# Optimization experiments

Measured on AMD Instinct MI355X. Metric: run time of the kernel, lower is better.

Reference implementation:

```python
import jax, jax.numpy as jnp
import numpy as np

N_NODES = 100000
N_EDGES = 1600000
IN_DIM, HID_DIM, OUT_DIM = 128, 128, 1


def gcn_conv(x, W, b, src, dst, n_nodes):
    """PyG-style GCNConv: add self-loops, symmetric D^-1/2 (A+I) D^-1/2 normalization.

    x: [N, F_in], W: [F_in, F_out], b: [F_out], src/dst: [E] int edge endpoints.
    """
    h = x @ W  # [N, F_out] transform first (as PyG does)
    # degree on A + I, counted over destination (symmetric graph assumption)
    ones = jnp.ones(src.shape[0], dtype=h.dtype)
    deg = jax.ops.segment_sum(ones, dst, num_segments=n_nodes) + 1.0  # +1 self loop
    dinv = jax.lax.rsqrt(deg)  # [N]
    norm = dinv[src] * dinv[dst]  # [E] edge normalization
    msg = h[src] * norm[:, None]  # [E, F_out] gather + scale
    agg = jax.ops.segment_sum(msg, dst, num_segments=n_nodes)  # scatter-add
    # self-loop contribution: norm_ii = dinv[i]^2
    out = agg + h * (dinv * dinv)[:, None]
    return out + b


def setup_inputs() -> dict:
    key = jax.random.key(0)
    k1, k2, k3, k4 = jax.random.split(key, 4)
    x = jax.random.normal(k1, (N_NODES, IN_DIM), dtype=jnp.float32)
    edge_index = jax.random.randint(k2, (2, N_EDGES), 0, N_NODES, dtype=jnp.int64)
    W1 = jax.random.normal(k3, (IN_DIM, HID_DIM), dtype=jnp.float32) * (1.0 / np.sqrt(IN_DIM))
    b1 = jnp.zeros((HID_DIM,), dtype=jnp.float32)
    W2 = jax.random.normal(k4, (HID_DIM, OUT_DIM), dtype=jnp.float32) * (1.0 / np.sqrt(HID_DIM))
    b2 = jnp.zeros((OUT_DIM,), dtype=jnp.float32)
    return {"x": x, "edge_index": edge_index, "W1": W1, "b1": b1, "W2": W2, "b2": b2}


def reference(x, edge_index, W1, b1, W2, b2):
    n = x.shape[0]
    src, dst = edge_index[0], edge_index[1]
    h = gcn_conv(x, W1, b1, src, dst, n)
    h = jax.nn.relu(h)
    # dropout(p=0.2) is identity at inference
    out = gcn_conv(h, W2, b2, src, dst, n)  # [N, 1]
    return out
```

## Files before the change

### kernel.cpp

```cpp
#include <hip/hip_runtime.h>

#define N_NODES 100000
#define N_EDGES 1600000
#define DIM 128

#define BSHIFT 8
#define BNODES 256
#define NBUCK 391
#define BCAP  4608
#define PCHUNK 4096
#define NB_PART ((N_EDGES + PCHUNK - 1) / PCHUNK)

#define GTILES 1563
#define GGRID  782

typedef short s16x8 __attribute__((ext_vector_type(8)));
typedef float f32x4 __attribute__((ext_vector_type(4)));

__device__ __forceinline__ unsigned short f2bf(float f) {
    unsigned u = __float_as_uint(f);
    u += 0x7fffu + ((u >> 16) & 1u);
    return (unsigned short)(u >> 16);
}
__device__ __forceinline__ float bflo(unsigned u) { return __uint_as_float(u << 16); }
__device__ __forceinline__ float bfhi(unsigned u) { return __uint_as_float(u & 0xffff0000u); }


__global__ void k_zero(int* __restrict__ gcur) {
    int t = blockIdx.x * blockDim.x + threadIdx.x;
    if (t < NBUCK) gcur[t] = t * BCAP;
}

__device__ __forceinline__ void part_body(char* smem, int bid,
                                          const int* __restrict__ src,
                                          const int* __restrict__ dst,
                                          int* __restrict__ gcur,
                                          int2* __restrict__ ebuf) {
    int* hist = (int*)smem;
    int* gbase = hist + NBUCK;
    int tid = threadIdx.x;
    long e0 = (long)bid * PCHUNK;
    int n = min(PCHUNK, (int)(N_EDGES - e0));
    for (int b = tid; b < NBUCK; b += 256) hist[b] = 0;
    __syncthreads();

    int mys[16], myd[16];
#pragma unroll
    for (int k = 0; k < 16; ++k) {
        int idx = k * 256 + tid;
        if (idx < n) {
            mys[k] = src[e0 + idx];
            myd[k] = dst[e0 + idx];
            atomicAdd(&hist[myd[k] >> BSHIFT], 1);
        } else {
            myd[k] = -1;
        }
    }
    __syncthreads();
    for (int b = tid; b < NBUCK; b += 256) {
        gbase[b] = hist[b] ? atomicAdd(&gcur[b], hist[b]) : 0;
        hist[b] = 0;
    }
    __syncthreads();
#pragma unroll
    for (int k = 0; k < 16; ++k) {
        if (myd[k] >= 0) {
            int b = myd[k] >> BSHIFT;
            int slot = gbase[b] + atomicAdd(&hist[b], 1);
            ebuf[slot] = make_int2(mys[k], myd[k]);
        }
    }
}

__device__ __forceinline__ void gemm_body(char* smem, int bid,
                                          const float* __restrict__ x,
                                          const float* __restrict__ W1,
                                          unsigned short* __restrict__ h1) {
    unsigned short* Wt = (unsigned short*)smem;
    int tid = threadIdx.x;
    for (int idx = tid; idx < DIM * DIM; idx += 256) {
        int k = idx >> 7, c = idx & 127;
        Wt[c * 128 + (k ^ ((c & 7) << 3))] = f2bf(W1[idx]);
    }
    __syncthreads();

    int wv = tid >> 6, lane = tid & 63;
    int g = lane >> 4, tl = lane & 15;
    unsigned short* cst = (unsigned short*)(smem + 32768 + wv * 4096);

    for (int tile = bid; tile < GTILES; tile += GGRID) {
        int rb = tile * 64 + wv * 16;
        if (rb >= N_NODES) continue;

        s16x8 afrag[4];
        const float* xrow = x + (size_t)(rb + tl) * DIM + g * 8;
#pragma unroll
        for (int kc = 0; kc < 4; ++kc) {
            float4 p0 = *(const float4*)(xrow + kc * 32);
            float4 p1 = *(const float4*)(xrow + kc * 32 + 4);
            s16x8 a;
            a[0] = (short)f2bf(p0.x); a[1] = (short)f2bf(p0.y);
            a[2] = (short)f2bf(p0.z); a[3] = (short)f2bf(p0.w);
            a[4] = (short)f2bf(p1.x); a[5] = (short)f2bf(p1.y);
            a[6] = (short)f2bf(p1.z); a[7] = (short)f2bf(p1.w);
            afrag[kc] = a;
        }

        f32x4 acc[8];
#pragma unroll
        for (int ct = 0; ct < 8; ++ct) acc[ct] = (f32x4)0.0f;
#pragma unroll
        for (int kc = 0; kc < 4; ++kc) {
#pragma unroll
            for (int ct = 0; ct < 8; ++ct) {
                int crow = ct * 16 + tl;
                int boff = crow * 256 + ((kc * 64 + g * 16) ^ ((crow & 7) << 4));
                s16x8 b = *(const s16x8*)((const char*)Wt + boff);
                acc[ct] = __builtin_amdgcn_mfma_f32_16x16x32_bf16(afrag[kc], b, acc[ct], 0, 0, 0);
            }
        }

#pragma unroll
        for (int ct = 0; ct < 8; ++ct) {
#pragma unroll
            for (int r = 0; r < 4; ++r) {
                float own = acc[ct][r];
                float oth = __shfl_xor(own, 1, 64);
                if ((lane & 1) == 0) {
                    unsigned pk = (unsigned)f2bf(own) | ((unsigned)f2bf(oth) << 16);
                    int row = g * 4 + r;
                    int col = ct * 16 + tl;
                    *(unsigned*)&cst[row * 128 + (col ^ (row << 3))] = pk;
                }
            }
        }
        asm volatile("s_waitcnt lgkmcnt(0)" ::: "memory");

        unsigned short* dstp = h1 + (size_t)rb * DIM;
#pragma unroll
        for (int c = 0; c < 4; ++c) {
            int row = c * 4 + g;
            uint4 v = *(const uint4*)&cst[row * 128 + ((tl ^ row) * 8)];
            *(uint4*)(dstp + c * 512 + lane * 8) = v;
        }
    }
}

__global__ __launch_bounds__(256) void k_part(const int* __restrict__ src,
                                              const int* __restrict__ dst,
                                              int* __restrict__ gcur,
                                              int2* __restrict__ ebuf) {
    __shared__ __align__(16) char smem[2 * NBUCK * 4 + 16];
    part_body(smem, blockIdx.x, src, dst, gcur, ebuf);
}

__global__ __launch_bounds__(256) void k_gemm(const float* __restrict__ x,
                                              const float* __restrict__ W1,
                                              unsigned short* __restrict__ h1) {
    __shared__ __align__(16) char smem[49152];
    gemm_body(smem, blockIdx.x, x, W1, h1);
}

__global__ __launch_bounds__(256) void k_pg(const int* __restrict__ src,
                                            const int* __restrict__ dst,
                                            int* __restrict__ gcur,
                                            int2* __restrict__ ebuf,
                                            const float* __restrict__ x,
                                            const float* __restrict__ W1,
                                            unsigned short* __restrict__ h1) {
    __shared__ __align__(16) char smem[49152];
    if (blockIdx.x < NB_PART) part_body(smem, blockIdx.x, src, dst, gcur, ebuf);
    else                      gemm_body(smem, blockIdx.x - NB_PART, x, W1, h1);
}

__global__ __launch_bounds__(256) void k_csrA(const int2* __restrict__ ebuf,
                                              const int* __restrict__ gcur,
                                              int* __restrict__ rp,
                                              int* __restrict__ cnt,
                                              float* __restrict__ dinv) {
    __shared__ int lcnt[BNODES];
    __shared__ int psum[BNODES];
    int b = blockIdx.x, t = threadIdx.x;
    int node0 = b << BSHIFT;
    lcnt[t] = 0;
    __syncthreads();
    int base = b * BCAP, end = gcur[b];
    for (int e = base + t; e < end; e += 256)
        atomicAdd(&lcnt[ebuf[e].y - node0], 1);
    __syncthreads();
    int c = lcnt[t];
    psum[t] = c;
    __syncthreads();
    for (int s = 1; s < 256; s <<= 1) {
        int u = (t >= s) ? psum[t - s] : 0;
        __syncthreads();
        psum[t] += u;
        __syncthreads();
    }
    int node = node0 + t;
    if (node < N_NODES) {
        rp[node] = base + psum[t] - c;
        cnt[node] = c;
        dinv[node] = rsqrtf((float)(c + 1));
    }
}

__global__ __launch_bounds__(256) void k_csrB(const int2* __restrict__ ebuf,
                                              const int* __restrict__ gcur,
                                              const int* __restrict__ rp,
                                              const float* __restrict__ dinv,
                                              int2* __restrict__ csrw) {
    __shared__ int lcur[BNODES];
    __shared__ float ldv[BNODES];
    int b = blockIdx.x, t = threadIdx.x;
    int node0 = b << BSHIFT;
    int base = b * BCAP, end = gcur[b];
    int node = node0 + t;
    if (node < N_NODES) { lcur[t] = rp[node] - base; ldv[t] = dinv[node]; }
    __syncthreads();
    int e = base + t;
    for (; e + 256 < end; e += 512) {
        int2 d0 = ebuf[e];
        int2 d1 = ebuf[e + 256];
        int l0 = d0.y - node0, l1 = d1.y - node0;
        float w0 = dinv[d0.x] * ldv[l0];
        float w1 = dinv[d1.x] * ldv[l1];
        int p0 = atomicAdd(&lcur[l0], 1);
        int p1 = atomicAdd(&lcur[l1], 1);
        csrw[base + p0] = make_int2(d0.x, __float_as_int(w0));
        csrw[base + p1] = make_int2(d1.x, __float_as_int(w1));
    }
    if (e < end) {
        int2 d0 = ebuf[e];
        int l0 = d0.y - node0;
        float w0 = dinv[d0.x] * ldv[l0];
        int p0 = atomicAdd(&lcur[l0], 1);
        csrw[base + p0] = make_int2(d0.x, __float_as_int(w0));
    }
}


__global__ __launch_bounds__(256) void k_agg1(const unsigned short* __restrict__ h1,
                                              const float* __restrict__ dinv,
                                              const int* __restrict__ rp,
                                              const int* __restrict__ cnt,
                                              const int2* __restrict__ csrw,
                                              const float* __restrict__ b1,
                                              const float* __restrict__ W2,
                                              float* __restrict__ z) {
    int lane = threadIdx.x & 63;
    int wv = threadIdx.x >> 6;
    int g = lane >> 4, tl = lane & 15;
    int i = blockIdx.x * 16 + wv * 4 + g;
    int c0 = tl * 8;
    float di = dinv[i];
    int beg = rp[i], end = beg + cnt[i];
    float a0 = 0.f, a1 = 0.f, a2 = 0.f, a3 = 0.f, a4 = 0.f, a5 = 0.f, a6 = 0.f, a7 = 0.f;
    const unsigned short* hbase = h1 + c0;

    int j = beg;
    for (; j + 4 <= end; j += 4) {
        int2 e0 = csrw[j];
        int2 e1 = csrw[j + 1];
        int2 e2 = csrw[j + 2];
        int2 e3 = csrw[j + 3];
        uint4 v0 = *(const uint4*)(hbase + (size_t)e0.x * DIM);
        uint4 v1 = *(const uint4*)(hbase + (size_t)e1.x * DIM);
        uint4 v2 = *(const uint4*)(hbase + (size_t)e2.x * DIM);
        uint4 v3 = *(const uint4*)(hbase + (size_t)e3.x * DIM);
        float w0 = __int_as_float(e0.y), w1 = __int_as_float(e1.y);
        float w2 = __int_as_float(e2.y), w3 = __int_as_float(e3.y);
        a0 = fmaf(bflo(v0.x), w0, a0); a1 = fmaf(bfhi(v0.x), w0, a1);
        a2 = fmaf(bflo(v0.y), w0, a2); a3 = fmaf(bfhi(v0.y), w0, a3);
        a4 = fmaf(bflo(v0.z), w0, a4); a5 = fmaf(bfhi(v0.z), w0, a5);
        a6 = fmaf(bflo(v0.w), w0, a6); a7 = fmaf(bfhi(v0.w), w0, a7);
        a0 = fmaf(bflo(v1.x), w1, a0); a1 = fmaf(bfhi(v1.x), w1, a1);
        a2 = fmaf(bflo(v1.y), w1, a2); a3 = fmaf(bfhi(v1.y), w1, a3);
        a4 = fmaf(bflo(v1.z), w1, a4); a5 = fmaf(bfhi(v1.z), w1, a5);
        a6 = fmaf(bflo(v1.w), w1, a6); a7 = fmaf(bfhi(v1.w), w1, a7);
        a0 = fmaf(bflo(v2.x), w2, a0); a1 = fmaf(bfhi(v2.x), w2, a1);
        a2 = fmaf(bflo(v2.y), w2, a2); a3 = fmaf(bfhi(v2.y), w2, a3);
        a4 = fmaf(bflo(v2.z), w2, a4); a5 = fmaf(bfhi(v2.z), w2, a5);
        a6 = fmaf(bflo(v2.w), w2, a6); a7 = fmaf(bfhi(v2.w), w2, a7);
        a0 = fmaf(bflo(v3.x), w3, a0); a1 = fmaf(bfhi(v3.x), w3, a1);
        a2 = fmaf(bflo(v3.y), w3, a2); a3 = fmaf(bfhi(v3.y), w3, a3);
        a4 = fmaf(bflo(v3.z), w3, a4); a5 = fmaf(bfhi(v3.z), w3, a5);
        a6 = fmaf(bflo(v3.w), w3, a6); a7 = fmaf(bfhi(v3.w), w3, a7);
    }
    for (; j < end; ++j) {
        int2 e0 = csrw[j];
        uint4 v0 = *(const uint4*)(hbase + (size_t)e0.x * DIM);
        float w0 = __int_as_float(e0.y);
        a0 = fmaf(bflo(v0.x), w0, a0); a1 = fmaf(bfhi(v0.x), w0, a1);
        a2 = fmaf(bflo(v0.y), w0, a2); a3 = fmaf(bfhi(v0.y), w0, a3);
        a4 = fmaf(bflo(v0.z), w0, a4); a5 = fmaf(bfhi(v0.z), w0, a5);
        a6 = fmaf(bflo(v0.w), w0, a6); a7 = fmaf(bfhi(v0.w), w0, a7);
    }

    uint4 vs = *(const uint4*)(hbase + (size_t)i * DIM);
    float sii = di * di;
    float4 bA = *(const float4*)(b1 + c0);
    float4 bB = *(const float4*)(b1 + c0 + 4);
    float4 wA = *(const float4*)(W2 + c0);
    float4 wB = *(const float4*)(W2 + c0 + 4);
    float p = 0.f;
    p += fmaxf(fmaf(bflo(vs.x), sii, a0) + bA.x, 0.f) * wA.x;
    p += fmaxf(fmaf(bfhi(vs.x), sii, a1) + bA.y, 0.f) * wA.y;
    p += fmaxf(fmaf(bflo(vs.y), sii, a2) + bA.z, 0.f) * wA.z;
    p += fmaxf(fmaf(bfhi(vs.y), sii, a3) + bA.w, 0.f) * wA.w;
    p += fmaxf(fmaf(bflo(vs.z), sii, a4) + bB.x, 0.f) * wB.x;
    p += fmaxf(fmaf(bfhi(vs.z), sii, a5) + bB.y, 0.f) * wB.y;
    p += fmaxf(fmaf(bflo(vs.w), sii, a6) + bB.z, 0.f) * wB.z;
    p += fmaxf(fmaf(bfhi(vs.w), sii, a7) + bB.w, 0.f) * wB.w;
#pragma unroll
    for (int off = 8; off >= 1; off >>= 1) p += __shfl_xor(p, off, 64);
    if (tl == 0) z[i] = p;
}


__global__ __launch_bounds__(256) void k_agg2(const float* __restrict__ zin,
                                              const float* __restrict__ dinv,
                                              const int* __restrict__ rp,
                                              const int* __restrict__ cnt,
                                              const int2* __restrict__ csrw,
                                              const float* __restrict__ b2,
                                              float* __restrict__ out) {
    int i = blockIdx.x * blockDim.x + threadIdx.x;
    if (i >= N_NODES) return;
    float di = dinv[i];
    int beg = rp[i], end = beg + cnt[i];
    float acc = 0.f;
    int j = beg;
    for (; j + 4 <= end; j += 4) {
        int2 e0 = csrw[j], e1 = csrw[j + 1], e2 = csrw[j + 2], e3 = csrw[j + 3];
        float z0 = zin[e0.x], z1 = zin[e1.x], z2 = zin[e2.x], z3 = zin[e3.x];
        acc = fmaf(z0, __int_as_float(e0.y), acc);
        acc = fmaf(z1, __int_as_float(e1.y), acc);
        acc = fmaf(z2, __int_as_float(e2.y), acc);
        acc = fmaf(z3, __int_as_float(e3.y), acc);
    }
    for (; j < end; ++j) {
        int2 e = csrw[j];
        acc = fmaf(zin[e.x], __int_as_float(e.y), acc);
    }
    out[i] = acc + zin[i] * di * di + b2[0];
}


extern "C" void kernel_launch(void* const* d_in, const int* in_sizes, int n_in,
                              void* d_out, int out_size, void* d_ws, size_t ws_size,
                              hipStream_t stream) {
    const float* x  = (const float*)d_in[0];
    const int*   ei = (const int*)d_in[1];
    const float* W1 = (const float*)d_in[2];
    const float* b1 = (const float*)d_in[3];
    const float* W2 = (const float*)d_in[4];
    const float* b2 = (const float*)d_in[5];
    float* out = (float*)d_out;

    const int* src = ei;
    const int* dst = ei + N_EDGES;

    char* ws = (char*)d_ws;
    size_t o = 0;
    auto take = [&](size_t bytes) { char* p = ws + o; o += (bytes + 255) & ~(size_t)255; return p; };
    int*   cnt   = (int*)take(sizeof(int) * N_NODES);
    int*   rp    = (int*)take(sizeof(int) * N_NODES);
    int*   gcur  = (int*)take(sizeof(int) * (NBUCK + 1));
    float* dinv  = (float*)take(sizeof(float) * N_NODES);
    float* z     = (float*)take(sizeof(float) * N_NODES);
    int2*  csrw  = (int2*)take(sizeof(int2) * (size_t)NBUCK * BCAP);
    unsigned short* h1 = (unsigned short*)take(sizeof(unsigned short) * (size_t)N_NODES * DIM);
    int2* ebuf_sep = (int2*)take(sizeof(int2) * (size_t)NBUCK * BCAP);
    bool fused = (o <= ws_size);
    int2* ebuf = fused ? ebuf_sep : (int2*)h1;

    const int NB_N = (N_NODES + 255) / 256;

    k_zero<<<2, 256, 0, stream>>>(gcur);
    if (fused) {
        k_pg<<<NB_PART + GGRID, 256, 0, stream>>>(src, dst, gcur, ebuf, x, W1, h1);
        k_csrA<<<NBUCK, 256, 0, stream>>>(ebuf, gcur, rp, cnt, dinv);
        k_csrB<<<NBUCK, 256, 0, stream>>>(ebuf, gcur, rp, dinv, csrw);
    } else {
        k_part<<<NB_PART, 256, 0, stream>>>(src, dst, gcur, ebuf);
        k_csrA<<<NBUCK, 256, 0, stream>>>(ebuf, gcur, rp, cnt, dinv);
        k_csrB<<<NBUCK, 256, 0, stream>>>(ebuf, gcur, rp, dinv, csrw);
        k_gemm<<<GGRID, 256, 0, stream>>>(x, W1, h1);
    }
    k_agg1<<<N_NODES / 16, 256, 0, stream>>>(h1, dinv, rp, cnt, csrw, b1, W2, z);
    k_agg2<<<NB_N, 256, 0, stream>>>(z, dinv, rp, cnt, csrw, b2, out);
}
```

Before: 145.8 us.

## Slice h1 into 8 feature slices for cache-resident aggregation

```diff
diff --git a/kernel.cpp b/kernel.cpp
--- a/kernel.cpp
+++ b/kernel.cpp
@@ -10,6 +10,9 @@
 #define BCAP  4608
 #define PCHUNK 4096
 #define NB_PART ((N_EDGES + PCHUNK - 1) / PCHUNK)
+
+#define NSLICE 8
+#define SLICE_ELEMS ((size_t)N_NODES * 16)
 
 #define GTILES 1563
 #define GGRID  782
@@ -75,7 +78,7 @@
 __device__ __forceinline__ void gemm_body(char* smem, int bid,
                                           const float* __restrict__ x,
                                           const float* __restrict__ W1,
-                                          unsigned short* __restrict__ h1) {
+                                          unsigned short* __restrict__ h1s) {
     unsigned short* Wt = (unsigned short*)smem;
     int tid = threadIdx.x;
     for (int idx = tid; idx < DIM * DIM; idx += 256) {
@@ -87,6 +90,8 @@
     int wv = tid >> 6, lane = tid & 63;
     int g = lane >> 4, tl = lane & 15;
     unsigned short* cst = (unsigned short*)(smem + 32768 + wv * 4096);
+
+    int s2 = tl >> 1, hh = tl & 1;
 
     for (int tile = bid; tile < GTILES; tile += GGRID) {
         int rb = tile * 64 + wv * 16;
@@ -136,12 +141,12 @@
         }
         asm volatile("s_waitcnt lgkmcnt(0)" ::: "memory");
 
-        unsigned short* dstp = h1 + (size_t)rb * DIM;
 #pragma unroll
         for (int c = 0; c < 4; ++c) {
             int row = c * 4 + g;
             uint4 v = *(const uint4*)&cst[row * 128 + ((tl ^ row) * 8)];
-            *(uint4*)(dstp + c * 512 + lane * 8) = v;
+            size_t n = (size_t)(rb + row);
+            *(uint4*)(h1s + (size_t)s2 * SLICE_ELEMS + n * 16 + hh * 8) = v;
         }
     }
 }
@@ -156,9 +161,9 @@
 
 __global__ __launch_bounds__(256) void k_gemm(const float* __restrict__ x,
                                               const float* __restrict__ W1,
-                                              unsigned short* __restrict__ h1) {
+                                              unsigned short* __restrict__ h1s) {
     __shared__ __align__(16) char smem[49152];
-    gemm_body(smem, blockIdx.x, x, W1, h1);
+    gemm_body(smem, blockIdx.x, x, W1, h1s);
 }
 
 __global__ __launch_bounds__(256) void k_pg(const int* __restrict__ src,
@@ -167,10 +172,10 @@
                                             int2* __restrict__ ebuf,
                                             const float* __restrict__ x,
                                             const float* __restrict__ W1,
-                                            unsigned short* __restrict__ h1) {
+                                            unsigned short* __restrict__ h1s) {
     __shared__ __align__(16) char smem[49152];
     if (blockIdx.x < NB_PART) part_body(smem, blockIdx.x, src, dst, gcur, ebuf);
-    else                      gemm_body(smem, blockIdx.x - NB_PART, x, W1, h1);
+    else                      gemm_body(smem, blockIdx.x - NB_PART, x, W1, h1s);
 }
 
 __global__ __launch_bounds__(256) void k_csrA(const int2* __restrict__ ebuf,
@@ -240,81 +245,81 @@
 }
 
 
-__global__ __launch_bounds__(256) void k_agg1(const unsigned short* __restrict__ h1,
-                                              const float* __restrict__ dinv,
-                                              const int* __restrict__ rp,
-                                              const int* __restrict__ cnt,
-                                              const int2* __restrict__ csrw,
-                                              const float* __restrict__ b1,
-                                              const float* __restrict__ W2,
-                                              float* __restrict__ z) {
+__global__ __launch_bounds__(256) void k_agg1s(const unsigned short* __restrict__ h1s,
+                                               const float* __restrict__ dinv,
+                                               const int* __restrict__ rp,
+                                               const int* __restrict__ cnt,
+                                               const int2* __restrict__ csrw,
+                                               const float* __restrict__ b1,
+                                               const float* __restrict__ W2,
+                                               float* __restrict__ zpart) {
+    int s = blockIdx.x & 7;
+    int tile0 = blockIdx.x >> 3;
     int lane = threadIdx.x & 63;
     int wv = threadIdx.x >> 6;
     int g = lane >> 4, tl = lane & 15;
-    int i = blockIdx.x * 16 + wv * 4 + g;
-    int c0 = tl * 8;
-    float di = dinv[i];
-    int beg = rp[i], end = beg + cnt[i];
-    float a0 = 0.f, a1 = 0.f, a2 = 0.f, a3 = 0.f, a4 = 0.f, a5 = 0.f, a6 = 0.f, a7 = 0.f;
-    const unsigned short* hbase = h1 + c0;
-
-    int j = beg;
-    for (; j + 4 <= end; j += 4) {
-        int2 e0 = csrw[j];
-        int2 e1 = csrw[j + 1];
-        int2 e2 = csrw[j + 2];
-        int2 e3 = csrw[j + 3];
-        uint4 v0 = *(const uint4*)(hbase + (size_t)e0.x * DIM);
-        uint4 v1 = *(const uint4*)(hbase + (size_t)e1.x * DIM);
-        uint4 v2 = *(const uint4*)(hbase + (size_t)e2.x * DIM);
-        uint4 v3 = *(const uint4*)(hbase + (size_t)e3.x * DIM);
-        float w0 = __int_as_float(e0.y), w1 = __int_as_float(e1.y);
-        float w2 = __int_as_float(e2.y), w3 = __int_as_float(e3.y);
-        a0 = fmaf(bflo(v0.x), w0, a0); a1 = fmaf(bfhi(v0.x), w0, a1);
-        a2 = fmaf(bflo(v0.y), w0, a2); a3 = fmaf(bfhi(v0.y), w0, a3);
-        a4 = fmaf(bflo(v0.z), w0, a4); a5 = fmaf(bfhi(v0.z), w0, a5);
-        a6 = fmaf(bflo(v0.w), w0, a6); a7 = fmaf(bfhi(v0.w), w0, a7);
-        a0 = fmaf(bflo(v1.x), w1, a0); a1 = fmaf(bfhi(v1.x), w1, a1);
-        a2 = fmaf(bflo(v1.y), w1, a2); a3 = fmaf(bfhi(v1.y), w1, a3);
-        a4 = fmaf(bflo(v1.z), w1, a4); a5 = fmaf(bfhi(v1.z), w1, a5);
-        a6 = fmaf(bflo(v1.w), w1, a6); a7 = fmaf(bfhi(v1.w), w1, a7);
-        a0 = fmaf(bflo(v2.x), w2, a0); a1 = fmaf(bfhi(v2.x), w2, a1);
-        a2 = fmaf(bflo(v2.y), w2, a2); a3 = fmaf(bfhi(v2.y), w2, a3);
-        a4 = fmaf(bflo(v2.z), w2, a4); a5 = fmaf(bfhi(v2.z), w2, a5);
-        a6 = fmaf(bflo(v2.w), w2, a6); a7 = fmaf(bfhi(v2.w), w2, a7);
-        a0 = fmaf(bflo(v3.x), w3, a0); a1 = fmaf(bfhi(v3.x), w3, a1);
-        a2 = fmaf(bflo(v3.y), w3, a2); a3 = fmaf(bfhi(v3.y), w3, a3);
-        a4 = fmaf(bflo(v3.z), w3, a4); a5 = fmaf(bfhi(v3.z), w3, a5);
-        a6 = fmaf(bflo(v3.w), w3, a6); a7 = fmaf(bfhi(v3.w), w3, a7);
-    }
-    for (; j < end; ++j) {
-        int2 e0 = csrw[j];
-        uint4 v0 = *(const uint4*)(hbase + (size_t)e0.x * DIM);
-        float w0 = __int_as_float(e0.y);
-        a0 = fmaf(bflo(v0.x), w0, a0); a1 = fmaf(bfhi(v0.x), w0, a1);
-        a2 = fmaf(bflo(v0.y), w0, a2); a3 = fmaf(bfhi(v0.y), w0, a3);
-        a4 = fmaf(bflo(v0.z), w0, a4); a5 = fmaf(bfhi(v0.z), w0, a5);
-        a6 = fmaf(bflo(v0.w), w0, a6); a7 = fmaf(bfhi(v0.w), w0, a7);
-    }
-
-    uint4 vs = *(const uint4*)(hbase + (size_t)i * DIM);
-    float sii = di * di;
-    float4 bA = *(const float4*)(b1 + c0);
-    float4 bB = *(const float4*)(b1 + c0 + 4);
-    float4 wA = *(const float4*)(W2 + c0);
-    float4 wB = *(const float4*)(W2 + c0 + 4);
-    float p = 0.f;
-    p += fmaxf(fmaf(bflo(vs.x), sii, a0) + bA.x, 0.f) * wA.x;
-    p += fmaxf(fmaf(bfhi(vs.x), sii, a1) + bA.y, 0.f) * wA.y;
-    p += fmaxf(fmaf(bflo(vs.y), sii, a2) + bA.z, 0.f) * wA.z;
-    p += fmaxf(fmaf(bfhi(vs.y), sii, a3) + bA.w, 0.f) * wA.w;
-    p += fmaxf(fmaf(bflo(vs.z), sii, a4) + bB.x, 0.f) * wB.x;
-    p += fmaxf(fmaf(bfhi(vs.z), sii, a5) + bB.y, 0.f) * wB.y;
-    p += fmaxf(fmaf(bflo(vs.w), sii, a6) + bB.z, 0.f) * wB.z;
-    p += fmaxf(fmaf(bfhi(vs.w), sii, a7) + bB.w, 0.f) * wB.w;
-#pragma unroll
-    for (int off = 8; off >= 1; off >>= 1) p += __shfl_xor(p, off, 64);
-    if (tl == 0) z[i] = p;
+    int p = tl >> 1, h = tl & 1;
+    const unsigned short* hs = h1s + (size_t)s * SLICE_ELEMS;
+    int cb = s * 16 + h * 8;
+
+    float4 bA = *(const float4*)(b1 + cb);
+    float4 bB = *(const float4*)(b1 + cb + 4);
+    float4 wA = *(const float4*)(W2 + cb);
+    float4 wB = *(const float4*)(W2 + cb + 4);
+
+    for (int tile = tile0; tile < N_NODES / 16; tile += 256) {
+        int i = tile * 16 + wv * 4 + g;
+        float di = dinv[i];
+        int beg = rp[i], end = beg + cnt[i];
+        float a[8];
+#pragma unroll
+        for (int q = 0; q < 8; ++q) a[q] = 0.f;
+
+        for (int off = beg;; off += 8) {
+            int j = off + p;
+            bool pred = j < end;
+            if (!__any(pred)) break;
+            if (pred) {
+                int2 e = csrw[j];
+                uint4 v = *(const uint4*)(hs + (size_t)e.x * 16 + h * 8);
+                float w = __int_as_float(e.y);
+                a[0] = fmaf(bflo(v.x), w, a[0]); a[1] = fmaf(bfhi(v.x), w, a[1]);
+                a[2] = fmaf(bflo(v.y), w, a[2]); a[3] = fmaf(bfhi(v.y), w, a[3]);
+                a[4] = fmaf(bflo(v.z), w, a[4]); a[5] = fmaf(bfhi(v.z), w, a[5]);
+                a[6] = fmaf(bflo(v.w), w, a[6]); a[7] = fmaf(bfhi(v.w), w, a[7]);
+            }
+        }
+#pragma unroll
+        for (int o = 2; o <= 8; o <<= 1) {
+#pragma unroll
+            for (int q = 0; q < 8; ++q) a[q] += __shfl_xor(a[q], o, 64);
+        }
+        float part = 0.f;
+        if (p == 0) {
+            uint4 vs = *(const uint4*)(hs + (size_t)i * 16 + h * 8);
+            float sii = di * di;
+            part += fmaxf(fmaf(bflo(vs.x), sii, a[0]) + bA.x, 0.f) * wA.x;
+            part += fmaxf(fmaf(bfhi(vs.x), sii, a[1]) + bA.y, 0.f) * wA.y;
+            part += fmaxf(fmaf(bflo(vs.y), sii, a[2]) + bA.z, 0.f) * wA.z;
+            part += fmaxf(fmaf(bfhi(vs.y), sii, a[3]) + bA.w, 0.f) * wA.w;
+            part += fmaxf(fmaf(bflo(vs.z), sii, a[4]) + bB.x, 0.f) * wB.x;
+            part += fmaxf(fmaf(bfhi(vs.z), sii, a[5]) + bB.y, 0.f) * wB.y;
+            part += fmaxf(fmaf(bflo(vs.w), sii, a[6]) + bB.z, 0.f) * wB.z;
+            part += fmaxf(fmaf(bfhi(vs.w), sii, a[7]) + bB.w, 0.f) * wB.w;
+        }
+        part += __shfl_xor(part, 1, 64);
+        if (tl == 0) zpart[(size_t)s * N_NODES + i] = part;
+    }
+}
+
+__global__ void k_zred(const float* __restrict__ zpart, float* __restrict__ z) {
+    int i = blockIdx.x * blockDim.x + threadIdx.x;
+    if (i < N_NODES) {
+        float t = 0.f;
+#pragma unroll
+        for (int s = 0; s < NSLICE; ++s) t += zpart[(size_t)s * N_NODES + i];
+        z[i] = t;
+    }
 }
 
 
@@ -369,25 +374,27 @@
     int*   gcur  = (int*)take(sizeof(int) * (NBUCK + 1));
     float* dinv  = (float*)take(sizeof(float) * N_NODES);
     float* z     = (float*)take(sizeof(float) * N_NODES);
+    float* zpart = (float*)take(sizeof(float) * (size_t)NSLICE * N_NODES);
     int2*  csrw  = (int2*)take(sizeof(int2) * (size_t)NBUCK * BCAP);
-    unsigned short* h1 = (unsigned short*)take(sizeof(unsigned short) * (size_t)N_NODES * DIM);
+    unsigned short* h1s = (unsigned short*)take(sizeof(unsigned short) * (size_t)NSLICE * SLICE_ELEMS);
     int2* ebuf_sep = (int2*)take(sizeof(int2) * (size_t)NBUCK * BCAP);
     bool fused = (o <= ws_size);
-    int2* ebuf = fused ? ebuf_sep : (int2*)h1;
+    int2* ebuf = fused ? ebuf_sep : (int2*)h1s;
 
     const int NB_N = (N_NODES + 255) / 256;
 
     k_zero<<<2, 256, 0, stream>>>(gcur);
     if (fused) {
-        k_pg<<<NB_PART + GGRID, 256, 0, stream>>>(src, dst, gcur, ebuf, x, W1, h1);
+        k_pg<<<NB_PART + GGRID, 256, 0, stream>>>(src, dst, gcur, ebuf, x, W1, h1s);
         k_csrA<<<NBUCK, 256, 0, stream>>>(ebuf, gcur, rp, cnt, dinv);
         k_csrB<<<NBUCK, 256, 0, stream>>>(ebuf, gcur, rp, dinv, csrw);
     } else {
         k_part<<<NB_PART, 256, 0, stream>>>(src, dst, gcur, ebuf);
         k_csrA<<<NBUCK, 256, 0, stream>>>(ebuf, gcur, rp, cnt, dinv);
         k_csrB<<<NBUCK, 256, 0, stream>>>(ebuf, gcur, rp, dinv, csrw);
-        k_gemm<<<GGRID, 256, 0, stream>>>(x, W1, h1);
-    }
-    k_agg1<<<N_NODES / 16, 256, 0, stream>>>(h1, dinv, rp, cnt, csrw, b1, W2, z);
+        k_gemm<<<GGRID, 256, 0, stream>>>(x, W1, h1s);
+    }
+    k_agg1s<<<2048, 256, 0, stream>>>(h1s, dinv, rp, cnt, csrw, b1, W2, zpart);
+    k_zred<<<NB_N, 256, 0, stream>>>(zpart, z);
     k_agg2<<<NB_N, 256, 0, stream>>>(z, dinv, rp, cnt, csrw, b2, out);
 }
```

After: 181.7 us. +24.6%, slower.
